# Kernel tuning notes

Hardware: AMD Instinct MI355X
Metric: run time of the kernel (lower is better)

## Reference

```python
import jax, jax.numpy as jnp
import numpy as np

N, C, HD = 8192, 1024, 128

def setup_inputs() -> dict:
    key = jax.random.key(0)
    ks = jax.random.split(key, 9)
    def xavier(k, fan_in, fan_out):
        lim = float(np.sqrt(6.0 / (fan_in + fan_out)))
        return jax.random.uniform(k, (fan_out, fan_in), jnp.float32, -lim, lim)
    return {
        "x": jax.random.normal(ks[0], (N, C), jnp.float32),
        "Wq": xavier(ks[1], C, HD), "bq": jnp.zeros((HD,), jnp.float32),
        "Wk": xavier(ks[2], C, HD), "bk": jnp.zeros((HD,), jnp.float32),
        "Wv": xavier(ks[3], C, C),  "bv": jnp.zeros((C,), jnp.float32),
        "Wo": xavier(ks[4], C, C),  "bo": jnp.zeros((C,), jnp.float32),
    }

def reference(x, Wq, bq, Wk, bk, Wv, bv, Wo, bo):
    scale = HD ** -0.5
    q = x @ Wq.T + bq          # (N, HD)
    k = x @ Wk.T + bk          # (N, HD)
    v = x @ Wv.T + bv          # (N, C)
    scores = (q @ k.T) * scale # (N, N)
    attn = jax.nn.softmax(scores, axis=-1)
    out = attn @ v             # (N, C)
    return out @ Wo.T + bo
```

## Files before the change

### kernel.cpp

```cpp
#include <hip/hip_runtime.h>

#define NTOK 8192
#define CDIM 1024
#define HDIM 128

typedef __attribute__((ext_vector_type(8))) short short8;
typedef __attribute__((ext_vector_type(4))) float floatx4;
typedef __attribute__((ext_vector_type(16))) float floatx16;
typedef __attribute__((ext_vector_type(4))) unsigned short ushort4v;

__device__ inline unsigned short f2bf(float f) {
    union { float f; unsigned u; } v; v.f = f;
    unsigned r = v.u + 0x7fffu + ((v.u >> 16) & 1u);
    return (unsigned short)(r >> 16);
}
__device__ inline float bf2f(short s) {
    union { unsigned u; float f; } v;
    v.u = ((unsigned)(unsigned short)s) << 16;
    return v.f;
}
__device__ inline void async16(const unsigned short* g, short* l) {
    __builtin_amdgcn_global_load_lds(
        (const __attribute__((address_space(1))) unsigned*)g,
        (__attribute__((address_space(3))) unsigned*)l, 16, 0, 0);
}

__global__ void cast_f32_bf16(const float* __restrict__ in,
                              unsigned short* __restrict__ out, int n4) {
    int i = blockIdx.x * blockDim.x + threadIdx.x;
    if (i < n4) {
        float4 v = ((const float4*)in)[i];
        ushort4 o;
        o.x = f2bf(v.x); o.y = f2bf(v.y); o.z = f2bf(v.z); o.w = f2bf(v.w);
        ((ushort4*)out)[i] = o;
    }
}

template<int SWZ>
__global__ __launch_bounds__(256) void gemm_nt(
    const unsigned short* __restrict__ A, const unsigned short* __restrict__ W,
    const float* __restrict__ bias, unsigned short* __restrict__ out, int M, int N, int K)
{
    __shared__ short As[4][64][8];
    __shared__ short Ws[4][64][8];
    const int tid = threadIdx.x;
    const int wave = tid >> 6, lane = tid & 63;
    const int lr = lane & 15, lc = lane >> 4;
    const int m0 = blockIdx.x * 64, n0 = blockIdx.y * 64;

    floatx4 acc[4] = {};
    const int srow = tid >> 2, sch = tid & 3;
    const unsigned short* Ag = A + (long)(m0 + srow) * K + sch * 8;
    const unsigned short* Wg = W + (long)(n0 + srow) * K + sch * 8;

    for (int k0 = 0; k0 < K; k0 += 32) {
        *(short8*)&As[sch][srow][0] = *(const short8*)(Ag + k0);
        *(short8*)&Ws[sch][srow][0] = *(const short8*)(Wg + k0);
        __syncthreads();
        short8 a = *(short8*)&As[lc][wave * 16 + lr][0];
#pragma unroll
        for (int s = 0; s < 4; s++) {
            short8 b = *(short8*)&Ws[lc][s * 16 + lr][0];
            acc[s] = __builtin_amdgcn_mfma_f32_16x16x32_bf16(a, b, acc[s], 0, 0, 0);
        }
        __syncthreads();
    }

#pragma unroll
    for (int s = 0; s < 4; s++) {
        int h = n0 + s * 16 + lr;
        float bv = bias[h];
        int tok0 = m0 + wave * 16 + lc * 4;
#pragma unroll
        for (int r = 0; r < 4; r++) {
            int tok = tok0 + r;
            if (SWZ)
                out[(tok >> 5) * 4096 + (h >> 3) * 256 + (tok & 31) * 8 + (h & 7)] =
                    f2bf(acc[s][r] + bv);
            else
                out[(long)tok * N + h] = f2bf(acc[s][r] + bv);
        }
    }
}

template<int MODE>
__global__ __launch_bounds__(256) void gemm128_nt(
    const unsigned short* __restrict__ A, const unsigned short* __restrict__ W,
    const float* __restrict__ bias, void* __restrict__ out, int M, int N, int K)
{
    __shared__ short As[128][4][8];
    __shared__ short Ws[128][4][8];
    const int tid = threadIdx.x, wave = tid >> 6, lane = tid & 63;
    const int lr = lane & 15, lc = lane >> 4;
    const int wm = (wave >> 1) * 64, wn = (wave & 1) * 64;
    const int m0 = blockIdx.x * 128, n0 = blockIdx.y * 128;

    floatx4 acc[4][4] = {};

    const int srow = lane >> 2, sch = lane & 3;
    const unsigned short* Ag0 = A + (long)(m0 + wave * 32 + srow) * K + sch * 8;
    const unsigned short* Ag1 = Ag0 + (long)16 * K;
    const unsigned short* Wg0 = W + (long)(n0 + wave * 32 + srow) * K + sch * 8;
    const unsigned short* Wg1 = Wg0 + (long)16 * K;
    short* lA0 = &As[wave * 32][0][0];
    short* lA1 = &As[wave * 32 + 16][0][0];
    short* lW0 = &Ws[wave * 32][0][0];
    short* lW1 = &Ws[wave * 32 + 16][0][0];

    for (int k0 = 0; k0 < K; k0 += 32) {
        async16(Ag0 + k0, lA0);
        async16(Ag1 + k0, lA1);
        async16(Wg0 + k0, lW0);
        async16(Wg1 + k0, lW1);
        __syncthreads();
        short8 af[4], bfg[4];
#pragma unroll
        for (int i = 0; i < 4; i++) af[i]  = *(short8*)&As[wm + i * 16 + lr][lc][0];
#pragma unroll
        for (int j = 0; j < 4; j++) bfg[j] = *(short8*)&Ws[wn + j * 16 + lr][lc][0];
#pragma unroll
        for (int i = 0; i < 4; i++)
#pragma unroll
            for (int j = 0; j < 4; j++)
                acc[i][j] = __builtin_amdgcn_mfma_f32_16x16x32_bf16(af[i], bfg[j], acc[i][j], 0, 0, 0);
        __syncthreads();
    }

#pragma unroll
    for (int i = 0; i < 4; i++) {
        int t0 = m0 + wm + i * 16 + lc * 4;
#pragma unroll
        for (int j = 0; j < 4; j++) {
            int c = n0 + wn + j * 16 + lr;
            float bv = bias[c];
            if (MODE == 0) {
                float* o = (float*)out;
#pragma unroll
                for (int r = 0; r < 4; r++) o[(long)(t0 + r) * N + c] = acc[i][j][r] + bv;
            } else {
                unsigned short* o = (unsigned short*)out;
                ushort4 pk;
                pk.x = f2bf(acc[i][j][0] + bv); pk.y = f2bf(acc[i][j][1] + bv);
                pk.z = f2bf(acc[i][j][2] + bv); pk.w = f2bf(acc[i][j][3] + bv);
                long off = (long)(c >> 8) * 2097152 + (t0 >> 5) * 8192 +
                           ((t0 & 31) >> 3) * 2048 + (c & 255) * 8 + (t0 & 7);
                *(ushort4*)&o[off] = pk;
            }
        }
    }
}

__global__ __launch_bounds__(256, 2) void attn_pv(
    const unsigned short* __restrict__ qb, const unsigned short* __restrict__ ksw,
    const unsigned short* __restrict__ vsw,
    unsigned short* __restrict__ Oa, unsigned short* __restrict__ Ob,
    float* __restrict__ la, float* __restrict__ lb)
{
    __shared__ short Ks[2][16][32][8];
    __shared__ short Vs[2][4][256][8];

    const int tid = threadIdx.x, wave = tid >> 6, lane = tid & 63;
    const int l31 = lane & 31, h = lane >> 5;
    const int m0 = blockIdx.x * 128, cblk = blockIdx.y;
    const int mw = m0 + wave * 32;
    const int nt0 = blockIdx.z * 128;
    unsigned short* Op = blockIdx.z ? Ob : Oa;
    float* ls = blockIdx.z ? lb : la;
    const float cexp = (float)(0.08838834764831845 * 1.4426950408889634);

    short8 qf[8];
#pragma unroll
    for (int kk = 0; kk < 8; kk++)
        qf[kk] = *(const short8*)&qb[(mw + l31) * HDIM + kk * 16 + h * 8];

    floatx16 acc[8] = {};
    float lsum = 0.f;

    const unsigned short* kg[2];
    short* const klb = &Ks[0][0][0][0];
#pragma unroll
    for (int t = 0; t < 2; t++) kg[t] = ksw + (wave * 2 + t) * 512 + lane * 8;
    const unsigned short* vg[4];
    short* const vlb = &Vs[0][0][0][0];
#pragma unroll
    for (int t = 0; t < 4; t++)
        vg[t] = vsw + (long)cblk * 2097152 + (wave * 4 + t) * 512 + lane * 8;

    {
        long nt = nt0;
#pragma unroll
        for (int t = 0; t < 2; t++)
            async16(kg[t] + nt * 4096, klb + (wave * 2 + t) * 512);
#pragma unroll
        for (int t = 0; t < 4; t++)
            async16(vg[t] + nt * 8192, vlb + (wave * 4 + t) * 512);
    }

    for (int it = 0; it < 128; ++it) {
        const int buf = it & 1;
        __syncthreads();
        if (it + 1 < 128) {
            long nt = nt0 + it + 1;
#pragma unroll
            for (int t = 0; t < 2; t++)
                async16(kg[t] + nt * 4096, klb + (buf ^ 1) * 4096 + (wave * 2 + t) * 512);
#pragma unroll
            for (int t = 0; t < 4; t++)
                async16(vg[t] + nt * 8192,
                        vlb + (buf ^ 1) * 8192 + (wave * 4 + t) * 512);
        }

        floatx16 st = {};
        __builtin_amdgcn_s_setprio(1);
#pragma unroll
        for (int kk = 0; kk < 8; kk++) {
            short8 kf = *(short8*)&Ks[buf][kk * 2 + h][l31][0];
            st = __builtin_amdgcn_mfma_f32_32x32x16_bf16(kf, qf[kk], st, 0, 0, 0);
        }
        __builtin_amdgcn_s_setprio(0);

        unsigned pk0, pk1, pk2, pk3, pk4, pk5, pk6, pk7;
        {
            float p0, p1;
#define PK(I, DST) \
            p0 = __builtin_amdgcn_exp2f(st[2 * I] * cexp); \
            p1 = __builtin_amdgcn_exp2f(st[2 * I + 1] * cexp); \
            lsum += p0 + p1; \
            asm("v_cvt_pk_bf16_f32 %0, %1, %2" : "=v"(DST) : "v"(p0), "v"(p1));
            PK(0, pk0) PK(1, pk1) PK(2, pk2) PK(3, pk3)
            PK(4, pk4) PK(5, pk5) PK(6, pk6) PK(7, pk7)
#undef PK
        }
        asm("v_permlane32_swap_b32 %0, %1" : "+v"(pk0), "+v"(pk2));
        asm("v_permlane32_swap_b32 %0, %1" : "+v"(pk1), "+v"(pk3));
        asm("v_permlane32_swap_b32 %0, %1" : "+v"(pk4), "+v"(pk6));
        asm("v_permlane32_swap_b32 %0, %1" : "+v"(pk5), "+v"(pk7));
        union { unsigned u[4]; short8 s; } up0, up1;
        up0.u[0] = pk0; up0.u[1] = pk1; up0.u[2] = pk2; up0.u[3] = pk3;
        up1.u[0] = pk4; up1.u[1] = pk5; up1.u[2] = pk6; up1.u[3] = pk7;
        const short8 pa0 = up0.s, pa1 = up1.s;

        __builtin_amdgcn_s_setprio(1);
#pragma unroll
        for (int ct = 0; ct < 8; ct++) {
            short8 bv0 = *(short8*)&Vs[buf][h][ct * 32 + l31][0];
            short8 bv1 = *(short8*)&Vs[buf][2 + h][ct * 32 + l31][0];
            acc[ct] = __builtin_amdgcn_mfma_f32_32x32x16_bf16(pa0, bv0, acc[ct], 0, 0, 0);
            acc[ct] = __builtin_amdgcn_mfma_f32_32x32x16_bf16(pa1, bv1, acc[ct], 0, 0, 0);
        }
        __builtin_amdgcn_s_setprio(0);
    }

#pragma unroll
    for (int ct = 0; ct < 8; ct++) {
        int c = cblk * 256 + ct * 32 + l31;
#pragma unroll
        for (int r = 0; r < 16; r++) {
            int q = (r & 3) + 8 * (r >> 2) + 4 * h;
            Op[(long)(mw + q) * CDIM + c] = f2bf(acc[ct][r]);
        }
    }
    if (blockIdx.y == 0) {
        lsum += __shfl_xor(lsum, 32);
        if (lane < 32) ls[mw + lane] = lsum;
    }
}

__global__ __launch_bounds__(256) void combine_attn(
    const unsigned short* __restrict__ Oa, unsigned short* __restrict__ Ob,
    const float* __restrict__ la, const float* __restrict__ lb)
{
    int i = blockIdx.x * blockDim.x + threadIdx.x;
    int row = i >> 7;
    float inv = 1.0f / (la[row] + lb[row]);
    short8 a = ((const short8*)Oa)[i];
    short8 b = ((const short8*)Ob)[i];
    short8 o;
#pragma unroll
    for (int e = 0; e < 8; e++) o[e] = (short)f2bf((bf2f(a[e]) + bf2f(b[e])) * inv);
    ((short8*)Ob)[i] = o;
}

extern "C" void kernel_launch(void* const* d_in, const int* in_sizes, int n_in,
                              void* d_out, int out_size, void* d_ws, size_t ws_size,
                              hipStream_t stream) {
    const float* x  = (const float*)d_in[0];
    const float* Wq = (const float*)d_in[1];
    const float* bq = (const float*)d_in[2];
    const float* Wk = (const float*)d_in[3];
    const float* bk = (const float*)d_in[4];
    const float* Wv = (const float*)d_in[5];
    const float* bv = (const float*)d_in[6];
    const float* Wo = (const float*)d_in[7];
    const float* bo = (const float*)d_in[8];

    char* ws = (char*)d_ws;
    unsigned short* x_bf   = (unsigned short*)(ws + 0);
    unsigned short* wq_bf  = (unsigned short*)(ws + 16777216);
    unsigned short* wk_bf  = (unsigned short*)(ws + 17039360);
    unsigned short* wv_bf  = (unsigned short*)(ws + 17301504);
    unsigned short* wo_bf  = (unsigned short*)(ws + 19398656);
    unsigned short* q_bf   = (unsigned short*)(ws + 21495808);
    unsigned short* k_swz  = (unsigned short*)(ws + 23592960);
    unsigned short* v_swz  = (unsigned short*)(ws + 25690112);
    unsigned short* attn_bf= (unsigned short*)(ws + 42467328);
    float* lsum_a          = (float*)(ws + 59244544);
    float* lsum_b          = (float*)(ws + 59277312);

    cast_f32_bf16<<<8192, 256, 0, stream>>>(x,  x_bf,  2097152);
    cast_f32_bf16<<<128,  256, 0, stream>>>(Wq, wq_bf, 32768);
    cast_f32_bf16<<<128,  256, 0, stream>>>(Wk, wk_bf, 32768);
    cast_f32_bf16<<<1024, 256, 0, stream>>>(Wv, wv_bf, 262144);
    cast_f32_bf16<<<1024, 256, 0, stream>>>(Wo, wo_bf, 262144);

    gemm_nt<0><<<dim3(128, 2), 256, 0, stream>>>(x_bf, wq_bf, bq, q_bf, NTOK, HDIM, CDIM);
    gemm_nt<1><<<dim3(128, 2), 256, 0, stream>>>(x_bf, wk_bf, bk, k_swz, NTOK, HDIM, CDIM);
    gemm128_nt<2><<<dim3(64, 8), 256, 0, stream>>>(x_bf, wv_bf, bv, v_swz, NTOK, CDIM, CDIM);

    attn_pv<<<dim3(64, 4, 2), 256, 0, stream>>>(q_bf, k_swz, v_swz,
                                                x_bf, attn_bf, lsum_a, lsum_b);
    combine_attn<<<4096, 256, 0, stream>>>(x_bf, attn_bf, lsum_a, lsum_b);

    gemm128_nt<0><<<dim3(64, 8), 256, 0, stream>>>(attn_bf, wo_bf, bo, d_out, NTOK, CDIM, CDIM);
}
```

Measured before the change: 400.1 us.

## Triple-buffer K/V tiles in attention kernel with explicit vmcnt waits

The attention PV kernel moves from double to triple buffering of K and V tiles in LDS. It prefetches two tiles ahead and waits with an explicit s_waitcnt vmcnt(6) before a single barrier per iteration, so tile loads have more time to overlap with the MFMA work. The row-sum accumulation is also split into four independent partial sums to shorten the dependency chain. In exchange, LDS use per block rises by half, which may limit occupancy at two blocks per CU, and the hand-written waitcnt logic depends on the exact count of issued async loads.

```diff
diff --git a/kernel.cpp b/kernel.cpp
--- a/kernel.cpp
+++ b/kernel.cpp
@@ -7,7 +7,6 @@
 typedef __attribute__((ext_vector_type(8))) short short8;
 typedef __attribute__((ext_vector_type(4))) float floatx4;
 typedef __attribute__((ext_vector_type(16))) float floatx16;
-typedef __attribute__((ext_vector_type(4))) unsigned short ushort4v;
 
 __device__ inline unsigned short f2bf(float f) {
     union { float f; unsigned u; } v; v.f = f;
@@ -156,8 +155,8 @@
     unsigned short* __restrict__ Oa, unsigned short* __restrict__ Ob,
     float* __restrict__ la, float* __restrict__ lb)
 {
-    __shared__ short Ks[2][16][32][8];
-    __shared__ short Vs[2][4][256][8];
+    __shared__ short Ks[3][16][32][8];
+    __shared__ short Vs[3][4][256][8];
 
     const int tid = threadIdx.x, wave = tid >> 6, lane = tid & 63;
     const int l31 = lane & 31, h = lane >> 5;
@@ -174,47 +173,51 @@
         qf[kk] = *(const short8*)&qb[(mw + l31) * HDIM + kk * 16 + h * 8];
 
     floatx16 acc[8] = {};
-    float lsum = 0.f;
+    float ls0 = 0.f, ls1 = 0.f, ls2 = 0.f, ls3 = 0.f;
 
     const unsigned short* kg[2];
-    short* const klb = &Ks[0][0][0][0];
 #pragma unroll
     for (int t = 0; t < 2; t++) kg[t] = ksw + (wave * 2 + t) * 512 + lane * 8;
     const unsigned short* vg[4];
-    short* const vlb = &Vs[0][0][0][0];
 #pragma unroll
     for (int t = 0; t < 4; t++)
         vg[t] = vsw + (long)cblk * 2097152 + (wave * 4 + t) * 512 + lane * 8;
 
-    {
-        long nt = nt0;
-#pragma unroll
-        for (int t = 0; t < 2; t++)
-            async16(kg[t] + nt * 4096, klb + (wave * 2 + t) * 512);
-#pragma unroll
-        for (int t = 0; t < 4; t++)
-            async16(vg[t] + nt * 8192, vlb + (wave * 4 + t) * 512);
-    }
+    short* kr = &Ks[0][0][0][0];
+    short* kn = &Ks[1][0][0][0];
+    short* kw = &Ks[2][0][0][0];
+    short* vr = &Vs[0][0][0][0];
+    short* vn = &Vs[1][0][0][0];
+    short* vw = &Vs[2][0][0][0];
+
+#define STAGE(NT, KD, VD)                                               \
+    {                                                                   \
+        long nt_ = (NT);                                                \
+        async16(kg[0] + nt_ * 4096, (KD) + (wave * 2 + 0) * 512);       \
+        async16(kg[1] + nt_ * 4096, (KD) + (wave * 2 + 1) * 512);       \
+        async16(vg[0] + nt_ * 8192, (VD) + (wave * 4 + 0) * 512);       \
+        async16(vg[1] + nt_ * 8192, (VD) + (wave * 4 + 1) * 512);       \
+        async16(vg[2] + nt_ * 8192, (VD) + (wave * 4 + 2) * 512);       \
+        async16(vg[3] + nt_ * 8192, (VD) + (wave * 4 + 3) * 512);       \
+    }
+
+    STAGE(nt0, kr, vr);
+    STAGE(nt0 + 1, kn, vn);
 
     for (int it = 0; it < 128; ++it) {
-        const int buf = it & 1;
-        __syncthreads();
-        if (it + 1 < 128) {
-            long nt = nt0 + it + 1;
-#pragma unroll
-            for (int t = 0; t < 2; t++)
-                async16(kg[t] + nt * 4096, klb + (buf ^ 1) * 4096 + (wave * 2 + t) * 512);
-#pragma unroll
-            for (int t = 0; t < 4; t++)
-                async16(vg[t] + nt * 8192,
-                        vlb + (buf ^ 1) * 8192 + (wave * 4 + t) * 512);
-        }
+        if (it == 127) asm volatile("s_waitcnt vmcnt(0)" ::: "memory");
+        else           asm volatile("s_waitcnt vmcnt(6)" ::: "memory");
+        __builtin_amdgcn_sched_barrier(0);
+        __builtin_amdgcn_s_barrier();
+        __builtin_amdgcn_sched_barrier(0);
+        if (it + 2 < 128) STAGE(nt0 + it + 2, kw, vw);
+        __builtin_amdgcn_sched_barrier(0);
 
         floatx16 st = {};
         __builtin_amdgcn_s_setprio(1);
 #pragma unroll
         for (int kk = 0; kk < 8; kk++) {
-            short8 kf = *(short8*)&Ks[buf][kk * 2 + h][l31][0];
+            short8 kf = *(short8*)(kr + (kk * 2 + h) * 256 + l31 * 8);
             st = __builtin_amdgcn_mfma_f32_32x32x16_bf16(kf, qf[kk], st, 0, 0, 0);
         }
         __builtin_amdgcn_s_setprio(0);
@@ -222,13 +225,13 @@
         unsigned pk0, pk1, pk2, pk3, pk4, pk5, pk6, pk7;
         {
             float p0, p1;
-#define PK(I, DST) \
+#define PK(I, DST, LS) \
             p0 = __builtin_amdgcn_exp2f(st[2 * I] * cexp); \
             p1 = __builtin_amdgcn_exp2f(st[2 * I + 1] * cexp); \
-            lsum += p0 + p1; \
+            LS += p0 + p1; \
             asm("v_cvt_pk_bf16_f32 %0, %1, %2" : "=v"(DST) : "v"(p0), "v"(p1));
-            PK(0, pk0) PK(1, pk1) PK(2, pk2) PK(3, pk3)
-            PK(4, pk4) PK(5, pk5) PK(6, pk6) PK(7, pk7)
+            PK(0, pk0, ls0) PK(1, pk1, ls1) PK(2, pk2, ls2) PK(3, pk3, ls3)
+            PK(4, pk4, ls0) PK(5, pk5, ls1) PK(6, pk6, ls2) PK(7, pk7, ls3)
 #undef PK
         }
         asm("v_permlane32_swap_b32 %0, %1" : "+v"(pk0), "+v"(pk2));
@@ -243,13 +246,17 @@
         __builtin_amdgcn_s_setprio(1);
 #pragma unroll
         for (int ct = 0; ct < 8; ct++) {
-            short8 bv0 = *(short8*)&Vs[buf][h][ct * 32 + l31][0];
-            short8 bv1 = *(short8*)&Vs[buf][2 + h][ct * 32 + l31][0];
+            short8 bv0 = *(short8*)(vr + h * 2048 + (ct * 32 + l31) * 8);
+            short8 bv1 = *(short8*)(vr + (2 + h) * 2048 + (ct * 32 + l31) * 8);
             acc[ct] = __builtin_amdgcn_mfma_f32_32x32x16_bf16(pa0, bv0, acc[ct], 0, 0, 0);
             acc[ct] = __builtin_amdgcn_mfma_f32_32x32x16_bf16(pa1, bv1, acc[ct], 0, 0, 0);
         }
         __builtin_amdgcn_s_setprio(0);
-    }
+
+        short* t0 = kr; kr = kn; kn = kw; kw = t0;
+        short* t1 = vr; vr = vn; vn = vw; vw = t1;
+    }
+#undef STAGE
 
 #pragma unroll
     for (int ct = 0; ct < 8; ct++) {
@@ -261,6 +268,7 @@
         }
     }
     if (blockIdx.y == 0) {
+        float lsum = (ls0 + ls1) + (ls2 + ls3);
         lsum += __shfl_xor(lsum, 32);
         if (lane < 32) ls[mw + lane] = lsum;
     }
```

Result: no change. 396.1 us (-1.0%).
